# Kernel tuning notes

Measured on AMD Instinct MI355X. Metric: run time of the kernel, lower is better.

Reference implementation:

```python
import jax, jax.numpy as jnp
import numpy as np

N_NODES = 50000
N_EDGES = 800000
D_IN = 128
D_OUT = 128
N_GRAPHS = 512
N_CONVS = 5
EPS = 1e-5


def setup_inputs() -> dict:
    key = jax.random.key(0)
    ks = jax.random.split(key, 8)
    x = jax.random.normal(ks[0], (N_NODES, D_IN), dtype=jnp.float32)
    edge_index = jax.random.randint(ks[1], (2, N_EDGES), 0, N_NODES, dtype=jnp.int32)
    batch = jnp.sort(jax.random.randint(ks[2], (N_NODES,), 0, N_GRAPHS, dtype=jnp.int32))
    s = 1.0 / np.sqrt(D_IN)
    W_rel = jax.random.normal(ks[3], (N_CONVS, D_OUT, D_IN), dtype=jnp.float32) * s
    b_rel = jax.random.normal(ks[4], (N_CONVS, D_OUT), dtype=jnp.float32) * s
    W_root = jax.random.normal(ks[5], (N_CONVS, D_OUT, D_IN), dtype=jnp.float32) * s
    gamma = jnp.ones((D_OUT,), dtype=jnp.float32)
    beta = jnp.zeros((D_OUT,), dtype=jnp.float32)
    Wc = jax.random.normal(ks[6], (96, D_OUT), dtype=jnp.float32) * (1.0 / np.sqrt(D_OUT))
    bc = jax.random.normal(ks[7], (96,), dtype=jnp.float32) * (1.0 / np.sqrt(D_OUT))
    return {"x": x, "edge_index": edge_index, "batch": batch, "i": 0,
            "W_rel": W_rel, "b_rel": b_rel, "W_root": W_root,
            "gamma": gamma, "beta": beta, "Wc": Wc, "bc": bc}


def reference(x, edge_index, batch, i, W_rel, b_rel, W_root, gamma, beta, Wc, bc):
    # --- 5 GraphConv branches, summed. GraphConv: lin_rel(sum_{j->i} x_j) + lin_root(x).
    # Sum over the 5 convs commutes with the linears, so fold the weights first.
    src, dst = edge_index[0], edge_index[1]
    agg = jax.ops.segment_sum(x[src], dst, num_segments=N_NODES)  # [N, D_in]
    Wr = jnp.sum(W_rel, axis=0)   # [D_out, D_in]
    Wt = jnp.sum(W_root, axis=0)  # [D_out, D_in]
    br = jnp.sum(b_rel, axis=0)   # [D_out]
    h = agg @ Wr.T + x @ Wt.T + br  # [N, D_out]
    # --- NodeLevelBatchNorm (training: batch stats over all nodes, biased var)
    mean = jnp.mean(h, axis=0)
    var = jnp.mean((h - mean) ** 2, axis=0)
    h = gamma * (h - mean) * jax.lax.rsqrt(var + EPS) + beta
    # --- global max pool over graphs, relu, classifier (i=0 -> no-dropout branch)
    pooled = jax.ops.segment_max(h, batch, num_segments=N_GRAPHS)  # [G, D_out]
    pooled = jax.nn.relu(pooled)
    return pooled @ Wc.T + bc  # [G, 96]
```

## Files before the change

### kernel.cpp

```cpp
#include <hip/hip_runtime.h>

#define EPS 1e-5f

constexpr int NN = 50000, NE = 800000, DD = 128, NG = 512, NC = 5, NO = 96;
constexpr int MAXB = 8192;
constexpr int NBUCK = 196;

typedef __attribute__((ext_vector_type(8))) short bf16x8;
typedef __attribute__((ext_vector_type(4))) float f32x4;

constexpr size_t HB   = 0;
constexpr size_t XB   = (size_t)NN * DD / 2;
constexpr size_t WB   = XB + (size_t)NN * DD / 2;
constexpr size_t BRO  = WB + DD * 256 / 2;
constexpr size_t CSUM = BRO + DD;
constexpr size_t CSQ  = CSUM + DD;
constexpr size_t POOL = CSQ + DD;
constexpr size_t GCNT = POOL + (size_t)NG * DD;
constexpr size_t ZEND = GCNT + 256;
constexpr size_t ROFF = ZEND;
constexpr size_t BSTOR= ROFF + NN + 1;
constexpr size_t CSR16= BSTOR + (size_t)NBUCK*MAXB;

constexpr int XCAST_B = NN * DD / 4 / 256;
constexpr int FOLD_B  = DD * DD / 256;
constexpr int BUCK_B  = (NE + 4095) / 4096;

static __device__ __forceinline__ unsigned short f2b(float f) {
    unsigned int u = __float_as_uint(f);
    return (unsigned short)((u + 0x7FFFu + ((u >> 16) & 1u)) >> 16);
}
static __device__ __forceinline__ float b2f(unsigned short h) {
    return __uint_as_float(((unsigned int)h) << 16);
}

__global__ __launch_bounds__(256) void k_prep(const float* __restrict__ x,
                                              const float* __restrict__ Wrel,
                                              const float* __restrict__ brel,
                                              const float* __restrict__ Wroot,
                                              const int* __restrict__ ei,
                                              float* __restrict__ ws, int* __restrict__ wi) {
    __shared__ int lcnt[256];
    __shared__ int lbase[256];
    int b = blockIdx.x, t = threadIdx.x;
    if (b < XCAST_B) {
        int i = b * 256 + t;
        float4 v = ((const float4*)x)[i];
        ushort4 o = {f2b(v.x), f2b(v.y), f2b(v.z), f2b(v.w)};
        ((ushort4*)(ws + XB))[i] = o;
    } else if (b < XCAST_B + FOLD_B) {
        int idx = (b - XCAST_B) * 256 + t;
        int k = idx >> 7, o = idx & 127;
        float wr = 0.f, wt = 0.f;
        for (int c = 0; c < NC; ++c) {
            wr += Wrel [c*DD*DD + o*DD + k];
            wt += Wroot[c*DD*DD + o*DD + k];
        }
        unsigned short* wb = (unsigned short*)(ws + WB);
        wb[o*256 + k]       = f2b(wr);
        wb[o*256 + 128 + k] = f2b(wt);
        if (k == 0) {
            float bias = 0.f;
            for (int c = 0; c < NC; ++c) bias += brel[c*DD + o];
            ws[BRO + o] = bias;
        }
    } else {
        int bb = b - XCAST_B - FOLD_B;
        lcnt[t] = 0;
        __syncthreads();
        int val[16], krk[16];
        #pragma unroll
        for (int j = 0; j < 16; ++j) {
            int e = bb * 4096 + j * 256 + t;
            krk[j] = -1;
            if (e < NE) {
                int d = ei[NE + e], s = ei[e];
                int key = d >> 8;
                int r = atomicAdd(&lcnt[key], 1);
                val[j] = s | ((d & 255) << 16);
                krk[j] = (key << 16) | r;
            }
        }
        __syncthreads();
        if (t < NBUCK && lcnt[t] > 0)
            lbase[t] = atomicAdd(&wi[GCNT + t], lcnt[t]);
        __syncthreads();
        #pragma unroll
        for (int j = 0; j < 16; ++j) {
            if (krk[j] >= 0) {
                int key = krk[j] >> 16, r = krk[j] & 0xFFFF;
                int p = lbase[key] + r;
                if (p < MAXB) wi[BSTOR + (size_t)key * MAXB + p] = val[j];
            }
        }
    }
}

__global__ __launch_bounds__(256) void k_sort(int* __restrict__ wi) {
    __shared__ int eds[MAXB];
    __shared__ unsigned short srt[MAXB];
    __shared__ int cnt[256], cnt2[256], lscan[256], gall[256];
    int t = threadIdx.x, b = blockIdx.x;
    int g = wi[GCNT + t];
    gall[t] = g; lscan[t] = g; cnt[t] = 0;
    __syncthreads();
    for (int off = 1; off < 256; off <<= 1) {
        int u = (t >= off) ? gall[t - off] : 0;
        __syncthreads();
        gall[t] += u;
        __syncthreads();
    }
    int base = gall[b] - lscan[b];
    int C = lscan[b]; if (C > MAXB) C = MAXB;
    __syncthreads();
    for (int i = t; i < C; i += 256) {
        int v = wi[BSTOR + (size_t)b * MAXB + i];
        eds[i] = v;
        atomicAdd(&cnt[v >> 16], 1);
    }
    __syncthreads();
    int cv = cnt[t];
    for (int off = 1; off < 256; off <<= 1) {
        int u = (t >= off) ? cnt[t - off] : 0;
        __syncthreads();
        cnt[t] += u;
        __syncthreads();
    }
    lscan[t] = cnt[t] - cv;
    cnt2[t] = 0;
    __syncthreads();
    int n = b * 256 + t;
    if (n < NN) wi[ROFF + n] = base + lscan[t];
    if (b == 0 && t == 0) wi[ROFF + NN] = NE;
    for (int i = t; i < C; i += 256) {
        int v = eds[i], k = v >> 16;
        int p = lscan[k] + atomicAdd(&cnt2[k], 1);
        srt[p] = (unsigned short)(v & 0xFFFF);
    }
    __syncthreads();
    unsigned short* csr = (unsigned short*)(wi + CSR16);
    for (int i = t; i < C; i += 256)
        csr[base + i] = srt[i];
}

__global__ __launch_bounds__(256) void k_gather(const int* __restrict__ wi,
                                                float* __restrict__ ws) {
    const unsigned short* xb = (const unsigned short*)(ws + XB);
    const unsigned short* csr = (const unsigned short*)(wi + CSR16);
    unsigned short* hb = (unsigned short*)(ws + HB);
    int tid = threadIdx.x;
    int n   = blockIdx.x * 16 + (tid >> 4);
    int sub = tid & 15;
    int c8  = sub * 8;
    if (n >= NN) return;
    int e0 = wi[ROFF + n], e1 = wi[ROFF + n + 1];
    int cnt = e1 - e0;
    float acc[8] = {};
    for (int base = 0; base < cnt; base += 16) {
        int myE = (base + sub < cnt) ? (int)csr[e0 + base + sub] : 0;
        int m = cnt - base; if (m > 16) m = 16;
        for (int j = 0; j < m; ++j) {
            int s = __shfl(myE, j, 16);
            bf16x8 v = *(const bf16x8*)&xb[(size_t)s * DD + c8];
            #pragma unroll
            for (int c = 0; c < 8; ++c) acc[c] += b2f((unsigned short)v[c]);
        }
    }
    bf16x8 o;
    #pragma unroll
    for (int c = 0; c < 8; ++c) o[c] = (short)f2b(acc[c]);
    *(bf16x8*)&hb[(size_t)n * DD + c8] = o;
}

__global__ __launch_bounds__(256) void k_gemm(float* __restrict__ ws) {
    __shared__ float sSum[128], sSq[128];
    const unsigned short* hb = (const unsigned short*)(ws + HB);
    const unsigned short* xb = (const unsigned short*)(ws + XB);
    const unsigned short* wb = (const unsigned short*)(ws + WB);
    unsigned short* hbo = (unsigned short*)(ws + HB);
    int tid  = threadIdx.x;
    if (tid < 128) { sSum[tid] = 0.f; sSq[tid] = 0.f; }
    int wave = tid >> 6, lane = tid & 63;
    int ch = wave & 1, rg = wave >> 1;
    int quad = lane >> 4, l16 = lane & 15;
    bf16x8 bf[4][8];
    #pragma unroll
    for (int nt = 0; nt < 4; ++nt)
        #pragma unroll
        for (int kt = 0; kt < 8; ++kt)
            bf[nt][kt] = *(const bf16x8*)(wb + (size_t)(ch*64 + nt*16 + l16)*256 + kt*32 + quad*8);
    float bias[4], csum[4] = {}, csq[4] = {};
    #pragma unroll
    for (int nt = 0; nt < 4; ++nt) bias[nt] = ws[BRO + ch*64 + nt*16 + l16];
    #pragma unroll
    for (int c = 0; c < 4; ++c) {
        int row0 = blockIdx.x * 128 + rg * 64 + c * 16;
        int arow = row0 + l16; if (arow > NN - 1) arow = NN - 1;
        const unsigned short* aggRow = hb + (size_t)arow * DD;
        const unsigned short* xRow   = xb + (size_t)arow * DD;
        bf16x8 af[8];
        #pragma unroll
        for (int kt = 0; kt < 8; ++kt)
            af[kt] = *(const bf16x8*)((kt < 4 ? aggRow + kt*32 : xRow + kt*32 - 128) + quad*8);
        __syncthreads();
        f32x4 acc[4] = {};
        #pragma unroll
        for (int kt = 0; kt < 8; ++kt)
            #pragma unroll
            for (int nt = 0; nt < 4; ++nt)
                acc[nt] = __builtin_amdgcn_mfma_f32_16x16x32_bf16(af[kt], bf[nt][kt], acc[nt], 0, 0, 0);
        #pragma unroll
        for (int nt = 0; nt < 4; ++nt) {
            int col = ch*64 + nt*16 + l16;
            #pragma unroll
            for (int r = 0; r < 4; ++r) {
                int row = row0 + quad*4 + r;
                float v = acc[nt][r] + bias[nt];
                if (row < NN) {
                    hbo[(size_t)row * DD + col] = f2b(v);
                    csum[nt] += v; csq[nt] += v * v;
                }
            }
        }
    }
    #pragma unroll
    for (int nt = 0; nt < 4; ++nt) {
        int col = ch*64 + nt*16 + l16;
        float cs = csum[nt], cq = csq[nt];
        cs += __shfl_xor(cs, 16); cs += __shfl_xor(cs, 32);
        cq += __shfl_xor(cq, 16); cq += __shfl_xor(cq, 32);
        if (quad == 0) { atomicAdd(&sSum[col], cs); atomicAdd(&sSq[col], cq); }
    }
    __syncthreads();
    if (tid < 128) {
        atomicAdd(&ws[CSUM + tid], sSum[tid]);
        atomicAdd(&ws[CSQ  + tid], sSq[tid]);
    }
}

__global__ __launch_bounds__(64) void k_pool(const int* __restrict__ batch,
                                             const float* __restrict__ gamma,
                                             const float* __restrict__ beta,
                                             float* __restrict__ ws) {
    int t  = threadIdx.x;
    int c0 = t * 2, c1 = c0 + 1;
    float mean0 = ws[CSUM + c0] * (1.0f / NN), mean1 = ws[CSUM + c1] * (1.0f / NN);
    float var0  = ws[CSQ + c0] * (1.0f / NN) - mean0 * mean0;
    float var1  = ws[CSQ + c1] * (1.0f / NN) - mean1 * mean1;
    float sc0 = gamma[c0] * rsqrtf(var0 + EPS), sc1 = gamma[c1] * rsqrtf(var1 + EPS);
    float sh0 = beta[c0] - sc0 * mean0,         sh1 = beta[c1] - sc1 * mean1;
    int n0 = blockIdx.x * 64;
    int n1 = n0 + 64; if (n1 > NN) n1 = NN;
    const unsigned int* hb32 = (const unsigned int*)ws;
    int cur = -1;
    float m0 = 0.f, m1 = 0.f;
    for (int n = n0; n < n1; ++n) {
        int g = batch[n];
        if (g != cur) {
            if (cur >= 0) {
                atomicMax((int*)&ws[POOL + (size_t)cur*DD + c0], __float_as_int(m0));
                atomicMax((int*)&ws[POOL + (size_t)cur*DD + c1], __float_as_int(m1));
            }
            cur = g; m0 = 0.f; m1 = 0.f;
        }
        unsigned int u = hb32[(size_t)n * 64 + t];
        float v0 = __uint_as_float(u << 16)          * sc0 + sh0;
        float v1 = __uint_as_float(u & 0xFFFF0000u)  * sc1 + sh1;
        m0 = fmaxf(m0, fmaxf(v0, 0.f));
        m1 = fmaxf(m1, fmaxf(v1, 0.f));
    }
    if (cur >= 0) {
        atomicMax((int*)&ws[POOL + (size_t)cur*DD + c0], __float_as_int(m0));
        atomicMax((int*)&ws[POOL + (size_t)cur*DD + c1], __float_as_int(m1));
    }
}

__global__ void k_cls(const float* __restrict__ Wc, const float* __restrict__ bc,
                      const float* __restrict__ ws, float* __restrict__ out) {
    __shared__ float pS[128];
    int g = blockIdx.x, t = threadIdx.x;
    pS[t] = ws[POOL + (size_t)g*DD + t];
    __syncthreads();
    if (t < NO) {
        float acc = bc[t];
        #pragma unroll 8
        for (int k = 0; k < DD; ++k) acc += pS[k] * Wc[t*DD + k];
        out[g*NO + t] = acc;
    }
}

extern "C" void kernel_launch(void* const* d_in, const int* in_sizes, int n_in,
                              void* d_out, int out_size, void* d_ws, size_t ws_size,
                              hipStream_t stream) {
    const float* x     = (const float*)d_in[0];
    const int*   ei    = (const int*)  d_in[1];
    const int*   batch = (const int*)  d_in[2];
    const float* Wrel  = (const float*)d_in[4];
    const float* brel  = (const float*)d_in[5];
    const float* Wroot = (const float*)d_in[6];
    const float* gamma = (const float*)d_in[7];
    const float* beta  = (const float*)d_in[8];
    const float* Wc    = (const float*)d_in[9];
    const float* bc    = (const float*)d_in[10];
    float* ws  = (float*)d_ws;
    int*   wi  = (int*)d_ws;
    float* out = (float*)d_out;

    hipMemsetAsync(ws + CSUM, 0, (ZEND - CSUM) * sizeof(float), stream);

    k_prep  <<<XCAST_B + FOLD_B + BUCK_B, 256, 0, stream>>>(x, Wrel, brel, Wroot, ei, ws, wi);
    k_sort  <<<NBUCK, 256, 0, stream>>>(wi);
    k_gather<<<(NN + 15)/16, 256, 0, stream>>>(wi, ws);
    k_gemm  <<<(NN + 127)/128, 256, 0, stream>>>(ws);
    k_pool  <<<(NN + 63)/64, 64, 0, stream>>>(batch, gamma, beta, ws);
    k_cls   <<<NG, DD, 0, stream>>>(Wc, bc, ws, out);
}
```

Before: 203.1 us.

## Fuse segment-max pooling into GEMM epilogue and apply BatchNorm after pooling

```diff
diff --git a/kernel.cpp b/kernel.cpp
--- a/kernel.cpp
+++ b/kernel.cpp
@@ -32,6 +32,14 @@
 }
 static __device__ __forceinline__ float b2f(unsigned short h) {
     return __uint_as_float(((unsigned int)h) << 16);
+}
+static __device__ __forceinline__ unsigned fkey(float f) {
+    unsigned u = __float_as_uint(f);
+    return (u >> 31) ? ~u : (u | 0x80000000u);
+}
+static __device__ __forceinline__ float unfkey(unsigned k) {
+    unsigned u = (k & 0x80000000u) ? (k ^ 0x80000000u) : ~k;
+    return __uint_as_float(u);
 }
 
 __global__ __launch_bounds__(256) void k_prep(const float* __restrict__ x,
@@ -156,30 +164,51 @@
     int e0 = wi[ROFF + n], e1 = wi[ROFF + n + 1];
     int cnt = e1 - e0;
     float acc[8] = {};
-    for (int base = 0; base < cnt; base += 16) {
-        int myE = (base + sub < cnt) ? (int)csr[e0 + base + sub] : 0;
-        int m = cnt - base; if (m > 16) m = 16;
-        for (int j = 0; j < m; ++j) {
+    int base = 0;
+    for (; base + 16 <= cnt; base += 16) {
+        int myE = (int)csr[e0 + base + sub];
+        #pragma unroll
+        for (int j = 0; j < 16; ++j) {
             int s = __shfl(myE, j, 16);
             bf16x8 v = *(const bf16x8*)&xb[(size_t)s * DD + c8];
             #pragma unroll
             for (int c = 0; c < 8; ++c) acc[c] += b2f((unsigned short)v[c]);
         }
     }
+    int rem = cnt - base;
+    if (rem > 0) {
+        int myE = (sub < rem) ? (int)csr[e0 + base + sub] : 0;
+        for (int j = 0; j < rem; ++j) {
+            int s = __shfl(myE, j, 16);
+            bf16x8 v = *(const bf16x8*)&xb[(size_t)s * DD + c8];
+            #pragma unroll
+            for (int c = 0; c < 8; ++c) acc[c] += b2f((unsigned short)v[c]);
+        }
+    }
     bf16x8 o;
     #pragma unroll
     for (int c = 0; c < 8; ++c) o[c] = (short)f2b(acc[c]);
     *(bf16x8*)&hb[(size_t)n * DD + c8] = o;
 }
 
-__global__ __launch_bounds__(256) void k_gemm(float* __restrict__ ws) {
+__global__ __launch_bounds__(256) void k_gemm(const int* __restrict__ batch,
+                                              float* __restrict__ ws) {
     __shared__ float sSum[128], sSq[128];
+    __shared__ int batchS[128];
+    __shared__ unsigned maxS[32][128];
     const unsigned short* hb = (const unsigned short*)(ws + HB);
     const unsigned short* xb = (const unsigned short*)(ws + XB);
     const unsigned short* wb = (const unsigned short*)(ws + WB);
-    unsigned short* hbo = (unsigned short*)(ws + HB);
+    unsigned* poolU = (unsigned*)(ws + POOL);
     int tid  = threadIdx.x;
     if (tid < 128) { sSum[tid] = 0.f; sSq[tid] = 0.f; }
+    for (int i = tid; i < 32 * 128; i += 256) ((unsigned*)maxS)[i] = 0u;
+    if (tid < 128) {
+        int r = blockIdx.x * 128 + tid; if (r > NN - 1) r = NN - 1;
+        batchS[tid] = batch[r];
+    }
+    __syncthreads();
+    int gBase = batchS[0];
     int wave = tid >> 6, lane = tid & 63;
     int ch = wave & 1, rg = wave >> 1;
     int quad = lane >> 4, l16 = lane & 15;
@@ -194,7 +223,8 @@
     for (int nt = 0; nt < 4; ++nt) bias[nt] = ws[BRO + ch*64 + nt*16 + l16];
     #pragma unroll
     for (int c = 0; c < 4; ++c) {
-        int row0 = blockIdx.x * 128 + rg * 64 + c * 16;
+        int lbase = rg * 64 + c * 16;
+        int row0 = blockIdx.x * 128 + lbase;
         int arow = row0 + l16; if (arow > NN - 1) arow = NN - 1;
         const unsigned short* aggRow = hb + (size_t)arow * DD;
         const unsigned short* xRow   = xb + (size_t)arow * DD;
@@ -202,7 +232,6 @@
         #pragma unroll
         for (int kt = 0; kt < 8; ++kt)
             af[kt] = *(const bf16x8*)((kt < 4 ? aggRow + kt*32 : xRow + kt*32 - 128) + quad*8);
-        __syncthreads();
         f32x4 acc[4] = {};
         #pragma unroll
         for (int kt = 0; kt < 8; ++kt)
@@ -212,16 +241,36 @@
         #pragma unroll
         for (int nt = 0; nt < 4; ++nt) {
             int col = ch*64 + nt*16 + l16;
+            float mx = 0.f; int gcur = -1;
             #pragma unroll
             for (int r = 0; r < 4; ++r) {
                 int row = row0 + quad*4 + r;
-                float v = acc[nt][r] + bias[nt];
                 if (row < NN) {
-                    hbo[(size_t)row * DD + col] = f2b(v);
+                    float v = acc[nt][r] + bias[nt];
                     csum[nt] += v; csq[nt] += v * v;
+                    int g = batchS[lbase + quad*4 + r];
+                    if (g != gcur) {
+                        if (gcur >= 0) {
+                            int rel = gcur - gBase;
+                            if (rel < 32) atomicMax(&maxS[rel][col], fkey(mx));
+                            else atomicMax(&poolU[(size_t)gcur * DD + col], fkey(mx));
+                        }
+                        gcur = g; mx = v;
+                    } else mx = fmaxf(mx, v);
                 }
             }
-        }
+            if (gcur >= 0) {
+                int rel = gcur - gBase;
+                if (rel < 32) atomicMax(&maxS[rel][col], fkey(mx));
+                else atomicMax(&poolU[(size_t)gcur * DD + col], fkey(mx));
+            }
+        }
+    }
+    __syncthreads();
+    int span = batchS[127] - gBase + 1; if (span > 32) span = 32;
+    for (int i = tid; i < span * 128; i += 256) {
+        unsigned k = maxS[i >> 7][i & 127];
+        if (k) atomicMax(&poolU[(size_t)(gBase + (i >> 7)) * DD + (i & 127)], k);
     }
     #pragma unroll
     for (int nt = 0; nt < 4; ++nt) {
@@ -238,53 +287,27 @@
     }
 }
 
-__global__ __launch_bounds__(64) void k_pool(const int* __restrict__ batch,
-                                             const float* __restrict__ gamma,
+__global__ __launch_bounds__(128) void k_out(const float* __restrict__ gamma,
                                              const float* __restrict__ beta,
-                                             float* __restrict__ ws) {
-    int t  = threadIdx.x;
-    int c0 = t * 2, c1 = c0 + 1;
-    float mean0 = ws[CSUM + c0] * (1.0f / NN), mean1 = ws[CSUM + c1] * (1.0f / NN);
-    float var0  = ws[CSQ + c0] * (1.0f / NN) - mean0 * mean0;
-    float var1  = ws[CSQ + c1] * (1.0f / NN) - mean1 * mean1;
-    float sc0 = gamma[c0] * rsqrtf(var0 + EPS), sc1 = gamma[c1] * rsqrtf(var1 + EPS);
-    float sh0 = beta[c0] - sc0 * mean0,         sh1 = beta[c1] - sc1 * mean1;
-    int n0 = blockIdx.x * 64;
-    int n1 = n0 + 64; if (n1 > NN) n1 = NN;
-    const unsigned int* hb32 = (const unsigned int*)ws;
-    int cur = -1;
-    float m0 = 0.f, m1 = 0.f;
-    for (int n = n0; n < n1; ++n) {
-        int g = batch[n];
-        if (g != cur) {
-            if (cur >= 0) {
-                atomicMax((int*)&ws[POOL + (size_t)cur*DD + c0], __float_as_int(m0));
-                atomicMax((int*)&ws[POOL + (size_t)cur*DD + c1], __float_as_int(m1));
-            }
-            cur = g; m0 = 0.f; m1 = 0.f;
-        }
-        unsigned int u = hb32[(size_t)n * 64 + t];
-        float v0 = __uint_as_float(u << 16)          * sc0 + sh0;
-        float v1 = __uint_as_float(u & 0xFFFF0000u)  * sc1 + sh1;
-        m0 = fmaxf(m0, fmaxf(v0, 0.f));
-        m1 = fmaxf(m1, fmaxf(v1, 0.f));
-    }
-    if (cur >= 0) {
-        atomicMax((int*)&ws[POOL + (size_t)cur*DD + c0], __float_as_int(m0));
-        atomicMax((int*)&ws[POOL + (size_t)cur*DD + c1], __float_as_int(m1));
-    }
-}
-
-__global__ void k_cls(const float* __restrict__ Wc, const float* __restrict__ bc,
-                      const float* __restrict__ ws, float* __restrict__ out) {
+                                             const float* __restrict__ Wc,
+                                             const float* __restrict__ bc,
+                                             const float* __restrict__ ws,
+                                             float* __restrict__ out) {
     __shared__ float pS[128];
     int g = blockIdx.x, t = threadIdx.x;
-    pS[t] = ws[POOL + (size_t)g*DD + t];
+    float mean = ws[CSUM + t] * (1.0f / NN);
+    float var  = ws[CSQ + t] * (1.0f / NN) - mean * mean;
+    float sc   = gamma[t] * rsqrtf(var + EPS);
+    float sh   = beta[t] - sc * mean;
+    unsigned k = ((const unsigned*)(ws + POOL))[(size_t)g * DD + t];
+    float p = 0.f;
+    if (k) p = fmaxf(unfkey(k) * sc + sh, 0.f);
+    pS[t] = p;
     __syncthreads();
     if (t < NO) {
         float acc = bc[t];
         #pragma unroll 8
-        for (int k = 0; k < DD; ++k) acc += pS[k] * Wc[t*DD + k];
+        for (int kk = 0; kk < DD; ++kk) acc += pS[kk] * Wc[t*DD + kk];
         out[g*NO + t] = acc;
     }
 }
@@ -311,7 +334,6 @@
     k_prep  <<<XCAST_B + FOLD_B + BUCK_B, 256, 0, stream>>>(x, Wrel, brel, Wroot, ei, ws, wi);
     k_sort  <<<NBUCK, 256, 0, stream>>>(wi);
     k_gather<<<(NN + 15)/16, 256, 0, stream>>>(wi, ws);
-    k_gemm  <<<(NN + 127)/128, 256, 0, stream>>>(ws);
-    k_pool  <<<(NN + 63)/64, 64, 0, stream>>>(batch, gamma, beta, ws);
-    k_cls   <<<NG, DD, 0, stream>>>(Wc, bc, ws, out);
-}
+    k_gemm  <<<(NN + 127)/128, 256, 0, stream>>>(batch, ws);
+    k_out   <<<NG, 128, 0, stream>>>(gamma, beta, Wc, bc, ws, out);
+}
```

New measurement: 188.9 us. 1.08x faster.
